# Kernel optimization log

Hardware: AMD Instinct MI355X
Metric: run time of the kernel (lower is better)

The kernel has to match this reference:

```python
import jax, jax.numpy as jnp
import numpy as np

NUM_EXPERTS = 8
HIDDEN = 2048
INTER = 5504
TOKENS = 16384  # total permuted tokens across all experts


def setup_inputs() -> dict:
    key = jax.random.key(0)
    k0, k1, k2, k3 = jax.random.split(key, 4)
    scale = 0.02  # typical init std for llama-style projections
    permuted_local_hidden_states = jax.random.normal(k0, (TOKENS, HIDDEN), jnp.float32)
    gate_w = jax.random.normal(k1, (NUM_EXPERTS, HIDDEN, INTER), jnp.float32) * scale
    up_w = jax.random.normal(k2, (NUM_EXPERTS, HIDDEN, INTER), jnp.float32) * scale
    down_w = jax.random.normal(k3, (NUM_EXPERTS, INTER, HIDDEN), jnp.float32) * scale
    tokens_per_expert = jnp.full((NUM_EXPERTS,), TOKENS // NUM_EXPERTS, jnp.int32)
    return {
        "permuted_local_hidden_states": permuted_local_hidden_states,
        "gate_w": gate_w,
        "up_w": up_w,
        "down_w": down_w,
        "tokens_per_expert": tokens_per_expert,
    }


def reference(permuted_local_hidden_states, gate_w, up_w, down_w, tokens_per_expert):
    # tokens_per_expert is uniform (TOKENS // NUM_EXPERTS each), so the
    # sequential per-expert slice loop is exactly a grouped/batched GEMM:
    # reshape tokens into [E, T_e, H] and run all experts at once.
    E = gate_w.shape[0]
    H = permuted_local_hidden_states.shape[-1]
    x = permuted_local_hidden_states.reshape(E, -1, H)  # [E, T_e, H]
    g = jnp.einsum("eth,ehi->eti", x, gate_w)           # gate proj
    u = jnp.einsum("eth,ehi->eti", x, up_w)             # up proj
    h = jax.nn.silu(g) * u                               # SwiGLU
    out = jnp.einsum("eti,eih->eth", h, down_w)         # down proj
    return out.reshape(-1, H)
```

## Files before the change

kernel.cpp:

```cpp
#include <hip/hip_runtime.h>
#include <hip/hip_bf16.h>

#define NE 8
#define HID 2048
#define INTER 5504
#define TOK 16384
#define TE 2048

typedef __bf16 bf16x8 __attribute__((ext_vector_type(8)));
typedef float f32x4 __attribute__((ext_vector_type(4)));

__device__ __forceinline__ void async_copy16(const void* g, void* l) {
    __builtin_amdgcn_global_load_lds(
        (const __attribute__((address_space(1))) void*)g,
        (__attribute__((address_space(3))) void*)l,
        16, 0, 0);
}

__device__ __forceinline__ int chunk_swz(int q) { return q ^ ((q >> 3) & 7); }

struct alignas(8) bf4 { __hip_bfloat162 a, b; };

__global__ void cast_x_kernel(const float* __restrict__ in, __hip_bfloat16* __restrict__ out) {
    size_t i = (size_t)blockIdx.x * blockDim.x + threadIdx.x;
    float4 v = reinterpret_cast<const float4*>(in)[i];
    bf4 p;
    p.a.x = __float2bfloat16(v.x);
    p.a.y = __float2bfloat16(v.y);
    p.b.x = __float2bfloat16(v.z);
    p.b.y = __float2bfloat16(v.w);
    reinterpret_cast<bf4*>(out)[i] = p;
}

__global__ void tcast_kernel(const float* __restrict__ in, __hip_bfloat16* __restrict__ out,
                             int R, int C) {
    __shared__ float tile[32][33];
    const int e = blockIdx.z;
    const int r0 = blockIdx.y * 32, c0 = blockIdx.x * 32;
    const float* src = in + (size_t)e * R * C;
    __hip_bfloat16* dst = out + (size_t)e * R * C;
    const int tx = threadIdx.x;
    const int ty = threadIdx.y;
#pragma unroll
    for (int i = 0; i < 32; i += 8)
        tile[ty + i][tx] = src[(size_t)(r0 + ty + i) * C + (c0 + tx)];
    __syncthreads();
#pragma unroll
    for (int i = 0; i < 32; i += 8)
        dst[(size_t)(c0 + ty + i) * R + (r0 + tx)] = __float2bfloat16(tile[tx][ty + i]);
}

__global__ __launch_bounds__(256, 2) void gemm1_swiglu_kernel(
    const __hip_bfloat16* __restrict__ xb,
    const __hip_bfloat16* __restrict__ gwt,
    const __hip_bfloat16* __restrict__ uwt,
    __hip_bfloat16* __restrict__ hout) {
    const int e = blockIdx.z;
    const int mt = blockIdx.x;
    const int nt = blockIdx.y;
    const int m0 = mt * 128;
    const int n0 = nt * 128;

    const __hip_bfloat16* A = xb + (size_t)(e * TE + m0) * HID;
    const __hip_bfloat16* Bg = gwt + (size_t)e * INTER * HID + (size_t)n0 * HID;
    const __hip_bfloat16* Bu = uwt + (size_t)e * INTER * HID + (size_t)n0 * HID;

    __shared__ __align__(16) __hip_bfloat16 As[128 * 32];
    __shared__ __align__(16) __hip_bfloat16 Bgs[128 * 32];
    __shared__ __align__(16) __hip_bfloat16 Bus[128 * 32];

    const int tid = threadIdx.x;
    const int wave = tid >> 6, lane = tid & 63;
    const int ch0 = wave * 128 + lane;

    const int wm = (wave >> 1) * 64;
    const int wn = (wave & 1) * 64;
    const int qd = lane >> 4;
    const int ln = lane & 15;

    f32x4 accg[4][4], accu[4][4];
    const f32x4 z4 = {0.f, 0.f, 0.f, 0.f};
#pragma unroll
    for (int mi = 0; mi < 4; ++mi)
#pragma unroll
        for (int ni = 0; ni < 4; ++ni) { accg[mi][ni] = z4; accu[mi][ni] = z4; }

    for (int kk = 0; kk < HID; kk += 32) {
#pragma unroll
        for (int i = 0; i < 2; ++i) {
            const int c = ch0 + i * 64;
            const int id = chunk_swz(c);
            const int row = id >> 2;
            const int col = (id & 3) * 8;
            async_copy16(A + (size_t)row * HID + kk + col, (void*)(As + c * 8));
            async_copy16(Bg + (size_t)row * HID + kk + col, (void*)(Bgs + c * 8));
            async_copy16(Bu + (size_t)row * HID + kk + col, (void*)(Bus + c * 8));
        }
        __syncthreads();

        bf16x8 af[4], bgf[4], buf_[4];
#pragma unroll
        for (int mi = 0; mi < 4; ++mi) {
            const int p = chunk_swz((wm + mi * 16 + ln) * 4 + qd);
            af[mi] = *reinterpret_cast<const bf16x8*>(As + p * 8);
        }
#pragma unroll
        for (int ni = 0; ni < 4; ++ni) {
            const int p = chunk_swz((wn + ni * 16 + ln) * 4 + qd);
            bgf[ni] = *reinterpret_cast<const bf16x8*>(Bgs + p * 8);
            buf_[ni] = *reinterpret_cast<const bf16x8*>(Bus + p * 8);
        }
#pragma unroll
        for (int mi = 0; mi < 4; ++mi)
#pragma unroll
            for (int ni = 0; ni < 4; ++ni) {
                accg[mi][ni] = __builtin_amdgcn_mfma_f32_16x16x32_bf16(af[mi], bgf[ni], accg[mi][ni], 0, 0, 0);
                accu[mi][ni] = __builtin_amdgcn_mfma_f32_16x16x32_bf16(af[mi], buf_[ni], accu[mi][ni], 0, 0, 0);
            }
        __syncthreads();
    }

    __hip_bfloat16* Hbase = hout + (size_t)(e * TE + m0) * INTER + n0;
#pragma unroll
    for (int mi = 0; mi < 4; ++mi)
#pragma unroll
        for (int ni = 0; ni < 4; ++ni)
#pragma unroll
            for (int r = 0; r < 4; ++r) {
                const int rr = wm + mi * 16 + qd * 4 + r;
                const int cc = wn + ni * 16 + ln;
                const float g = accg[mi][ni][r];
                const float u = accu[mi][ni][r];
                const float s = g / (1.0f + __expf(-g));
                Hbase[(size_t)rr * INTER + cc] = __float2bfloat16(s * u);
            }
}

__global__ __launch_bounds__(256, 2) void gemm2_kernel(
    const __hip_bfloat16* __restrict__ hb,
    const __hip_bfloat16* __restrict__ dwt,
    float* __restrict__ out) {
    const int e = blockIdx.z;
    const int mt = blockIdx.x;
    const int nt = blockIdx.y;
    const int m0 = mt * 128;
    const int n0 = nt * 128;

    const __hip_bfloat16* A = hb + (size_t)(e * TE + m0) * INTER;
    const __hip_bfloat16* B = dwt + (size_t)e * HID * INTER + (size_t)n0 * INTER;

    __shared__ __align__(16) __hip_bfloat16 As[128 * 32];
    __shared__ __align__(16) __hip_bfloat16 Bs[128 * 32];

    const int tid = threadIdx.x;
    const int wave = tid >> 6, lane = tid & 63;
    const int ch0 = wave * 128 + lane;

    const int wm = (wave >> 1) * 64;
    const int wn = (wave & 1) * 64;
    const int qd = lane >> 4;
    const int ln = lane & 15;

    f32x4 acc[4][4];
    const f32x4 z4 = {0.f, 0.f, 0.f, 0.f};
#pragma unroll
    for (int mi = 0; mi < 4; ++mi)
#pragma unroll
        for (int ni = 0; ni < 4; ++ni) acc[mi][ni] = z4;

    for (int kk = 0; kk < INTER; kk += 32) {
#pragma unroll
        for (int i = 0; i < 2; ++i) {
            const int c = ch0 + i * 64;
            const int id = chunk_swz(c);
            const int row = id >> 2;
            const int col = (id & 3) * 8;
            async_copy16(A + (size_t)row * INTER + kk + col, (void*)(As + c * 8));
            async_copy16(B + (size_t)row * INTER + kk + col, (void*)(Bs + c * 8));
        }
        __syncthreads();

        bf16x8 af[4], bf_[4];
#pragma unroll
        for (int mi = 0; mi < 4; ++mi) {
            const int p = chunk_swz((wm + mi * 16 + ln) * 4 + qd);
            af[mi] = *reinterpret_cast<const bf16x8*>(As + p * 8);
        }
#pragma unroll
        for (int ni = 0; ni < 4; ++ni) {
            const int p = chunk_swz((wn + ni * 16 + ln) * 4 + qd);
            bf_[ni] = *reinterpret_cast<const bf16x8*>(Bs + p * 8);
        }
#pragma unroll
        for (int mi = 0; mi < 4; ++mi)
#pragma unroll
            for (int ni = 0; ni < 4; ++ni)
                acc[mi][ni] = __builtin_amdgcn_mfma_f32_16x16x32_bf16(af[mi], bf_[ni], acc[mi][ni], 0, 0, 0);
        __syncthreads();
    }

    float* Obase = out + (size_t)(e * TE + m0) * HID + n0;
#pragma unroll
    for (int mi = 0; mi < 4; ++mi)
#pragma unroll
        for (int ni = 0; ni < 4; ++ni)
#pragma unroll
            for (int r = 0; r < 4; ++r) {
                const int rr = wm + mi * 16 + qd * 4 + r;
                const int cc = wn + ni * 16 + ln;
                Obase[(size_t)rr * HID + cc] = acc[mi][ni][r];
            }
}

extern "C" void kernel_launch(void* const* d_in, const int* in_sizes, int n_in,
                              void* d_out, int out_size, void* d_ws, size_t ws_size,
                              hipStream_t stream) {
    const float* x = (const float*)d_in[0];
    const float* gw = (const float*)d_in[1];
    const float* uw = (const float*)d_in[2];
    const float* dw = (const float*)d_in[3];
    float* out = (float*)d_out;

    const size_t XB_BYTES = (size_t)TOK * HID * 2;
    const size_t WT_BYTES = (size_t)NE * INTER * HID * 2;
    char* ws = (char*)d_ws;
    __hip_bfloat16* xb = (__hip_bfloat16*)(ws);
    __hip_bfloat16* gwt = (__hip_bfloat16*)(ws + XB_BYTES);
    __hip_bfloat16* uwt = (__hip_bfloat16*)(ws + XB_BYTES + WT_BYTES);
    __hip_bfloat16* hb = (__hip_bfloat16*)(ws + XB_BYTES + 2 * WT_BYTES);
    __hip_bfloat16* dwt = gwt;

    cast_x_kernel<<<(TOK * HID) / (256 * 4), 256, 0, stream>>>(x, xb);
    tcast_kernel<<<dim3(INTER / 32, HID / 32, NE), dim3(32, 8), 0, stream>>>(gw, gwt, HID, INTER);
    tcast_kernel<<<dim3(INTER / 32, HID / 32, NE), dim3(32, 8), 0, stream>>>(uw, uwt, HID, INTER);
    gemm1_swiglu_kernel<<<dim3(TE / 128, INTER / 128, NE), 256, 0, stream>>>(xb, gwt, uwt, hb);
    tcast_kernel<<<dim3(HID / 32, INTER / 32, NE), dim3(32, 8), 0, stream>>>(dw, dwt, INTER, HID);
    gemm2_kernel<<<dim3(TE / 128, HID / 128, NE), 256, 0, stream>>>(hb, dwt, out);
}
```

Baseline: 2.435 ms.

## Rewrite GEMMs with 256x256 tiles, 4-stage LDS pipeline, tile swizzle, wider transpose-cast

Both GEMM kernels move to 512-thread blocks with larger 256-row tiles and a four-buffer async global-to-LDS pipeline that prefetches two K-steps ahead. Loads are split across two half-steps, with raw s_barrier plus waitcnt replacing __syncthreads, and setprio raised around the MFMA bursts. Block indices are remapped so consecutive workgroups cover the same expert and weight tile, aiming at better L2 reuse. The transpose-cast kernel now packs pairs of bf16 values and writes 16-byte vectors, cutting the cost of the weight conversion passes. Risks are higher register pressure from the larger accumulator sets and the correctness of the hand-tuned waitcnt and barrier placement.

```diff
diff --git a/kernel.cpp b/kernel.cpp
--- a/kernel.cpp
+++ b/kernel.cpp
@@ -18,6 +18,12 @@
 }
 
 __device__ __forceinline__ int chunk_swz(int q) { return q ^ ((q >> 3) & 7); }
+
+__device__ __forceinline__ void block_barrier() {
+    asm volatile("" ::: "memory");
+    __builtin_amdgcn_s_barrier();
+    asm volatile("" ::: "memory");
+}
 
 struct alignas(8) bf4 { __hip_bfloat162 a, b; };
 
@@ -32,183 +38,290 @@
     reinterpret_cast<bf4*>(out)[i] = p;
 }
 
-__global__ void tcast_kernel(const float* __restrict__ in, __hip_bfloat16* __restrict__ out,
-                             int R, int C) {
-    __shared__ float tile[32][33];
+__global__ __launch_bounds__(256) void tcast2_kernel(const float* __restrict__ in,
+                                                     __hip_bfloat16* __restrict__ out,
+                                                     int R, int C) {
+    __shared__ unsigned int D[32][129];
     const int e = blockIdx.z;
-    const int r0 = blockIdx.y * 32, c0 = blockIdx.x * 32;
+    const int r0 = blockIdx.y * 64, c0 = blockIdx.x * 128;
     const float* src = in + (size_t)e * R * C;
     __hip_bfloat16* dst = out + (size_t)e * R * C;
-    const int tx = threadIdx.x;
-    const int ty = threadIdx.y;
-#pragma unroll
-    for (int i = 0; i < 32; i += 8)
-        tile[ty + i][tx] = src[(size_t)(r0 + ty + i) * C + (c0 + tx)];
+    const int tid = threadIdx.x;
+
+#pragma unroll
+    for (int it = 0; it < 16; ++it) {
+        const int idx = tid + it * 256;
+        const int rp = idx >> 7, c = idx & 127;
+        const float lo = src[(size_t)(r0 + 2 * rp) * C + (c0 + c)];
+        const float hi = src[(size_t)(r0 + 2 * rp + 1) * C + (c0 + c)];
+        const unsigned short a = __builtin_bit_cast(unsigned short, __float2bfloat16(lo));
+        const unsigned short b = __builtin_bit_cast(unsigned short, __float2bfloat16(hi));
+        D[rp][c] = (unsigned)a | ((unsigned)b << 16);
+    }
     __syncthreads();
 #pragma unroll
-    for (int i = 0; i < 32; i += 8)
-        dst[(size_t)(c0 + ty + i) * R + (r0 + tx)] = __float2bfloat16(tile[tx][ty + i]);
-}
-
-__global__ __launch_bounds__(256, 2) void gemm1_swiglu_kernel(
+    for (int it = 0; it < 4; ++it) {
+        const int idx = tid + it * 256;
+        const int c = idx >> 3, q = idx & 7;
+        uint4 w;
+        w.x = D[4 * q + 0][c];
+        w.y = D[4 * q + 1][c];
+        w.z = D[4 * q + 2][c];
+        w.w = D[4 * q + 3][c];
+        *reinterpret_cast<uint4*>(dst + (size_t)(c0 + c) * R + r0 + q * 8) = w;
+    }
+}
+
+__global__ __launch_bounds__(512, 2) void gemm1_swiglu_kernel(
     const __hip_bfloat16* __restrict__ xb,
     const __hip_bfloat16* __restrict__ gwt,
     const __hip_bfloat16* __restrict__ uwt,
     __hip_bfloat16* __restrict__ hout) {
-    const int e = blockIdx.z;
-    const int mt = blockIdx.x;
-    const int nt = blockIdx.y;
-    const int m0 = mt * 128;
-    const int n0 = nt * 128;
+    const int lin = blockIdx.x + ((blockIdx.y + blockIdx.z * 43) << 3);
+    const int swz = (lin & 7) * 344 + (lin >> 3);
+    const int e = swz / 344;
+    const int rem = swz - e * 344;
+    const int nt = rem >> 3, mt = rem & 7;
+    const int m0 = mt * 256, n0 = nt * 128;
 
     const __hip_bfloat16* A = xb + (size_t)(e * TE + m0) * HID;
     const __hip_bfloat16* Bg = gwt + (size_t)e * INTER * HID + (size_t)n0 * HID;
     const __hip_bfloat16* Bu = uwt + (size_t)e * INTER * HID + (size_t)n0 * HID;
 
-    __shared__ __align__(16) __hip_bfloat16 As[128 * 32];
-    __shared__ __align__(16) __hip_bfloat16 Bgs[128 * 32];
-    __shared__ __align__(16) __hip_bfloat16 Bus[128 * 32];
+    __shared__ __align__(16) __hip_bfloat16 S[4 * 2048 * 8];
 
     const int tid = threadIdx.x;
     const int wave = tid >> 6, lane = tid & 63;
-    const int ch0 = wave * 128 + lane;
-
-    const int wm = (wave >> 1) * 64;
-    const int wn = (wave & 1) * 64;
-    const int qd = lane >> 4;
-    const int ln = lane & 15;
-
-    f32x4 accg[4][4], accu[4][4];
+    const int wmh = (wave >> 2) * 128;
+    const int wnq = (wave & 3) * 32;
+    const int qd = lane >> 4, ln = lane & 15;
+
+    const __hip_bfloat16* aSrc[2];
+    const __hip_bfloat16* bSrc[2];
+#pragma unroll
+    for (int p = 0; p < 2; ++p) {
+        const int c = p * 512 + tid;
+        const int id = chunk_swz(c);
+        const int row = id >> 2, col = (id & 3) * 8;
+        aSrc[p] = A + (size_t)row * HID + col;
+        bSrc[p] = (row < 128 ? Bg + (size_t)row * HID
+                             : Bu + (size_t)(row - 128) * HID) + col;
+    }
+
+    int pA[8], pG[2], pU[2];
+#pragma unroll
+    for (int mi = 0; mi < 8; ++mi) pA[mi] = chunk_swz((wmh + mi * 16 + ln) * 4 + qd);
+#pragma unroll
+    for (int ni = 0; ni < 2; ++ni) {
+        pG[ni] = 1024 + chunk_swz((wnq + ni * 16 + ln) * 4 + qd);
+        pU[ni] = 1024 + chunk_swz((128 + wnq + ni * 16 + ln) * 4 + qd);
+    }
+
+    f32x4 accg[8][2], accu[8][2];
     const f32x4 z4 = {0.f, 0.f, 0.f, 0.f};
 #pragma unroll
-    for (int mi = 0; mi < 4; ++mi)
-#pragma unroll
-        for (int ni = 0; ni < 4; ++ni) { accg[mi][ni] = z4; accu[mi][ni] = z4; }
-
-    for (int kk = 0; kk < HID; kk += 32) {
-#pragma unroll
-        for (int i = 0; i < 2; ++i) {
-            const int c = ch0 + i * 64;
-            const int id = chunk_swz(c);
-            const int row = id >> 2;
-            const int col = (id & 3) * 8;
-            async_copy16(A + (size_t)row * HID + kk + col, (void*)(As + c * 8));
-            async_copy16(Bg + (size_t)row * HID + kk + col, (void*)(Bgs + c * 8));
-            async_copy16(Bu + (size_t)row * HID + kk + col, (void*)(Bus + c * 8));
-        }
-        __syncthreads();
-
-        bf16x8 af[4], bgf[4], buf_[4];
-#pragma unroll
-        for (int mi = 0; mi < 4; ++mi) {
-            const int p = chunk_swz((wm + mi * 16 + ln) * 4 + qd);
-            af[mi] = *reinterpret_cast<const bf16x8*>(As + p * 8);
-        }
-#pragma unroll
-        for (int ni = 0; ni < 4; ++ni) {
-            const int p = chunk_swz((wn + ni * 16 + ln) * 4 + qd);
-            bgf[ni] = *reinterpret_cast<const bf16x8*>(Bgs + p * 8);
-            buf_[ni] = *reinterpret_cast<const bf16x8*>(Bus + p * 8);
-        }
-#pragma unroll
-        for (int mi = 0; mi < 4; ++mi)
-#pragma unroll
-            for (int ni = 0; ni < 4; ++ni) {
-                accg[mi][ni] = __builtin_amdgcn_mfma_f32_16x16x32_bf16(af[mi], bgf[ni], accg[mi][ni], 0, 0, 0);
-                accu[mi][ni] = __builtin_amdgcn_mfma_f32_16x16x32_bf16(af[mi], buf_[ni], accu[mi][ni], 0, 0, 0);
+    for (int mi = 0; mi < 8; ++mi)
+#pragma unroll
+        for (int ni = 0; ni < 2; ++ni) { accg[mi][ni] = z4; accu[mi][ni] = z4; }
+
+    const int NT = HID / 32;
+#pragma unroll
+    for (int t = 0; t < 2; ++t)
+#pragma unroll
+        for (int p = 0; p < 2; ++p) {
+            const int c = p * 512 + tid;
+            async_copy16(aSrc[p] + t * 32, (void*)(S + (size_t)(t * 2048 + c) * 8));
+            async_copy16(bSrc[p] + t * 32, (void*)(S + (size_t)(t * 2048 + 1024 + c) * 8));
+        }
+
+    for (int t = 0; t < NT; ++t) {
+        const __hip_bfloat16* Sb = S + (size_t)((t & 3) * 2048) * 8;
+        const int buf2 = ((t + 2) & 3) * 2048;
+        const int k2 = (t + 2 < NT ? t + 2 : t + 2 - NT) * 32;
+
+        {
+            const int c = tid;
+            async_copy16(aSrc[0] + k2, (void*)(S + (size_t)(buf2 + c) * 8));
+            async_copy16(bSrc[0] + k2, (void*)(S + (size_t)(buf2 + 1024 + c) * 8));
+        }
+        asm volatile("s_waitcnt vmcnt(6)" ::: "memory");
+        block_barrier();
+
+        bf16x8 bg[2], bu[2], af[4];
+#pragma unroll
+        for (int ni = 0; ni < 2; ++ni) {
+            bg[ni] = *reinterpret_cast<const bf16x8*>(Sb + (size_t)pG[ni] * 8);
+            bu[ni] = *reinterpret_cast<const bf16x8*>(Sb + (size_t)pU[ni] * 8);
+        }
+#pragma unroll
+        for (int mi = 0; mi < 4; ++mi)
+            af[mi] = *reinterpret_cast<const bf16x8*>(Sb + (size_t)pA[mi] * 8);
+
+        __builtin_amdgcn_s_setprio(1);
+#pragma unroll
+        for (int mi = 0; mi < 4; ++mi)
+#pragma unroll
+            for (int ni = 0; ni < 2; ++ni) {
+                accg[mi][ni] = __builtin_amdgcn_mfma_f32_16x16x32_bf16(af[mi], bg[ni], accg[mi][ni], 0, 0, 0);
+                accu[mi][ni] = __builtin_amdgcn_mfma_f32_16x16x32_bf16(af[mi], bu[ni], accu[mi][ni], 0, 0, 0);
             }
-        __syncthreads();
-    }
-
-    __hip_bfloat16* Hbase = hout + (size_t)(e * TE + m0) * INTER + n0;
-#pragma unroll
-    for (int mi = 0; mi < 4; ++mi)
-#pragma unroll
-        for (int ni = 0; ni < 4; ++ni)
+        __builtin_amdgcn_s_setprio(0);
+        block_barrier();
+
+        {
+            const int c = 512 + tid;
+            async_copy16(aSrc[1] + k2, (void*)(S + (size_t)(buf2 + c) * 8));
+            async_copy16(bSrc[1] + k2, (void*)(S + (size_t)(buf2 + 1024 + c) * 8));
+        }
+        bf16x8 af2[4];
+#pragma unroll
+        for (int mi = 0; mi < 4; ++mi)
+            af2[mi] = *reinterpret_cast<const bf16x8*>(Sb + (size_t)pA[mi + 4] * 8);
+
+        __builtin_amdgcn_s_setprio(1);
+#pragma unroll
+        for (int mi = 0; mi < 4; ++mi)
+#pragma unroll
+            for (int ni = 0; ni < 2; ++ni) {
+                accg[mi + 4][ni] = __builtin_amdgcn_mfma_f32_16x16x32_bf16(af2[mi], bg[ni], accg[mi + 4][ni], 0, 0, 0);
+                accu[mi + 4][ni] = __builtin_amdgcn_mfma_f32_16x16x32_bf16(af2[mi], bu[ni], accu[mi + 4][ni], 0, 0, 0);
+            }
+        __builtin_amdgcn_s_setprio(0);
+        block_barrier();
+    }
+
+    __hip_bfloat16* H = hout + (size_t)(e * TE + m0 + wmh) * INTER + n0 + wnq;
+#pragma unroll
+    for (int mi = 0; mi < 8; ++mi)
+#pragma unroll
+        for (int ni = 0; ni < 2; ++ni)
 #pragma unroll
             for (int r = 0; r < 4; ++r) {
-                const int rr = wm + mi * 16 + qd * 4 + r;
-                const int cc = wn + ni * 16 + ln;
+                const int rr = mi * 16 + qd * 4 + r;
+                const int cc = ni * 16 + ln;
                 const float g = accg[mi][ni][r];
                 const float u = accu[mi][ni][r];
                 const float s = g / (1.0f + __expf(-g));
-                Hbase[(size_t)rr * INTER + cc] = __float2bfloat16(s * u);
+                H[(size_t)rr * INTER + cc] = __float2bfloat16(s * u);
             }
 }
 
-__global__ __launch_bounds__(256, 2) void gemm2_kernel(
+__global__ __launch_bounds__(512, 2) void gemm2_kernel(
     const __hip_bfloat16* __restrict__ hb,
     const __hip_bfloat16* __restrict__ dwt,
     float* __restrict__ out) {
-    const int e = blockIdx.z;
-    const int mt = blockIdx.x;
-    const int nt = blockIdx.y;
-    const int m0 = mt * 128;
-    const int n0 = nt * 128;
+    const int lin = blockIdx.x + ((blockIdx.y + (blockIdx.z << 3)) << 3);
+    const int swz = (lin & 7) * 64 + (lin >> 3);
+    const int e = swz >> 6;
+    const int rem = swz & 63;
+    const int nt = rem >> 3, mt = rem & 7;
+    const int m0 = mt * 256, n0 = nt * 256;
 
     const __hip_bfloat16* A = hb + (size_t)(e * TE + m0) * INTER;
     const __hip_bfloat16* B = dwt + (size_t)e * HID * INTER + (size_t)n0 * INTER;
 
-    __shared__ __align__(16) __hip_bfloat16 As[128 * 32];
-    __shared__ __align__(16) __hip_bfloat16 Bs[128 * 32];
+    __shared__ __align__(16) __hip_bfloat16 S[4 * 2048 * 8];
 
     const int tid = threadIdx.x;
     const int wave = tid >> 6, lane = tid & 63;
-    const int ch0 = wave * 128 + lane;
-
-    const int wm = (wave >> 1) * 64;
-    const int wn = (wave & 1) * 64;
-    const int qd = lane >> 4;
-    const int ln = lane & 15;
-
-    f32x4 acc[4][4];
+    const int wmh = (wave >> 2) * 128;
+    const int wnq = (wave & 3) * 64;
+    const int qd = lane >> 4, ln = lane & 15;
+
+    const __hip_bfloat16* aSrc[2];
+    const __hip_bfloat16* bSrc[2];
+#pragma unroll
+    for (int p = 0; p < 2; ++p) {
+        const int c = p * 512 + tid;
+        const int id = chunk_swz(c);
+        const int row = id >> 2, col = (id & 3) * 8;
+        aSrc[p] = A + (size_t)row * INTER + col;
+        bSrc[p] = B + (size_t)row * INTER + col;
+    }
+
+    int pA[8], pB[4];
+#pragma unroll
+    for (int mi = 0; mi < 8; ++mi) pA[mi] = chunk_swz((wmh + mi * 16 + ln) * 4 + qd);
+#pragma unroll
+    for (int ni = 0; ni < 4; ++ni) pB[ni] = 1024 + chunk_swz((wnq + ni * 16 + ln) * 4 + qd);
+
+    f32x4 acc[8][4];
     const f32x4 z4 = {0.f, 0.f, 0.f, 0.f};
 #pragma unroll
-    for (int mi = 0; mi < 4; ++mi)
+    for (int mi = 0; mi < 8; ++mi)
 #pragma unroll
         for (int ni = 0; ni < 4; ++ni) acc[mi][ni] = z4;
 
-    for (int kk = 0; kk < INTER; kk += 32) {
-#pragma unroll
-        for (int i = 0; i < 2; ++i) {
-            const int c = ch0 + i * 64;
-            const int id = chunk_swz(c);
-            const int row = id >> 2;
-            const int col = (id & 3) * 8;
-            async_copy16(A + (size_t)row * INTER + kk + col, (void*)(As + c * 8));
-            async_copy16(B + (size_t)row * INTER + kk + col, (void*)(Bs + c * 8));
-        }
-        __syncthreads();
-
-        bf16x8 af[4], bf_[4];
-#pragma unroll
-        for (int mi = 0; mi < 4; ++mi) {
-            const int p = chunk_swz((wm + mi * 16 + ln) * 4 + qd);
-            af[mi] = *reinterpret_cast<const bf16x8*>(As + p * 8);
-        }
-#pragma unroll
-        for (int ni = 0; ni < 4; ++ni) {
-            const int p = chunk_swz((wn + ni * 16 + ln) * 4 + qd);
-            bf_[ni] = *reinterpret_cast<const bf16x8*>(Bs + p * 8);
-        }
+    const int NT = INTER / 32;
+#pragma unroll
+    for (int t = 0; t < 2; ++t)
+#pragma unroll
+        for (int p = 0; p < 2; ++p) {
+            const int c = p * 512 + tid;
+            async_copy16(aSrc[p] + t * 32, (void*)(S + (size_t)(t * 2048 + c) * 8));
+            async_copy16(bSrc[p] + t * 32, (void*)(S + (size_t)(t * 2048 + 1024 + c) * 8));
+        }
+
+    for (int t = 0; t < NT; ++t) {
+        const __hip_bfloat16* Sb = S + (size_t)((t & 3) * 2048) * 8;
+        const int buf2 = ((t + 2) & 3) * 2048;
+        const int k2 = (t + 2 < NT ? t + 2 : t + 2 - NT) * 32;
+
+        {
+            const int c = tid;
+            async_copy16(aSrc[0] + k2, (void*)(S + (size_t)(buf2 + c) * 8));
+            async_copy16(bSrc[0] + k2, (void*)(S + (size_t)(buf2 + 1024 + c) * 8));
+        }
+        asm volatile("s_waitcnt vmcnt(6)" ::: "memory");
+        block_barrier();
+
+        bf16x8 bf_[4], af[4];
+#pragma unroll
+        for (int ni = 0; ni < 4; ++ni)
+            bf_[ni] = *reinterpret_cast<const bf16x8*>(Sb + (size_t)pB[ni] * 8);
+#pragma unroll
+        for (int mi = 0; mi < 4; ++mi)
+            af[mi] = *reinterpret_cast<const bf16x8*>(Sb + (size_t)pA[mi] * 8);
+
+        __builtin_amdgcn_s_setprio(1);
 #pragma unroll
         for (int mi = 0; mi < 4; ++mi)
 #pragma unroll
             for (int ni = 0; ni < 4; ++ni)
                 acc[mi][ni] = __builtin_amdgcn_mfma_f32_16x16x32_bf16(af[mi], bf_[ni], acc[mi][ni], 0, 0, 0);
-        __syncthreads();
-    }
-
-    float* Obase = out + (size_t)(e * TE + m0) * HID + n0;
-#pragma unroll
-    for (int mi = 0; mi < 4; ++mi)
+        __builtin_amdgcn_s_setprio(0);
+        block_barrier();
+
+        {
+            const int c = 512 + tid;
+            async_copy16(aSrc[1] + k2, (void*)(S + (size_t)(buf2 + c) * 8));
+            async_copy16(bSrc[1] + k2, (void*)(S + (size_t)(buf2 + 1024 + c) * 8));
+        }
+        bf16x8 af2[4];
+#pragma unroll
+        for (int mi = 0; mi < 4; ++mi)
+            af2[mi] = *reinterpret_cast<const bf16x8*>(Sb + (size_t)pA[mi + 4] * 8);
+
+        __builtin_amdgcn_s_setprio(1);
+#pragma unroll
+        for (int mi = 0; mi < 4; ++mi)
+#pragma unroll
+            for (int ni = 0; ni < 4; ++ni)
+                acc[mi + 4][ni] = __builtin_amdgcn_mfma_f32_16x16x32_bf16(af2[mi], bf_[ni], acc[mi + 4][ni], 0, 0, 0);
+        __builtin_amdgcn_s_setprio(0);
+        block_barrier();
+    }
+
+    float* O = out + (size_t)(e * TE + m0 + wmh) * HID + n0 + wnq;
+#pragma unroll
+    for (int mi = 0; mi < 8; ++mi)
 #pragma unroll
         for (int ni = 0; ni < 4; ++ni)
 #pragma unroll
             for (int r = 0; r < 4; ++r) {
-                const int rr = wm + mi * 16 + qd * 4 + r;
-                const int cc = wn + ni * 16 + ln;
-                Obase[(size_t)rr * HID + cc] = acc[mi][ni][r];
+                const int rr = mi * 16 + qd * 4 + r;
+                const int cc = ni * 16 + ln;
+                O[(size_t)rr * HID + cc] = acc[mi][ni][r];
             }
 }
 
@@ -231,9 +344,9 @@
     __hip_bfloat16* dwt = gwt;
 
     cast_x_kernel<<<(TOK * HID) / (256 * 4), 256, 0, stream>>>(x, xb);
-    tcast_kernel<<<dim3(INTER / 32, HID / 32, NE), dim3(32, 8), 0, stream>>>(gw, gwt, HID, INTER);
-    tcast_kernel<<<dim3(INTER / 32, HID / 32, NE), dim3(32, 8), 0, stream>>>(uw, uwt, HID, INTER);
-    gemm1_swiglu_kernel<<<dim3(TE / 128, INTER / 128, NE), 256, 0, stream>>>(xb, gwt, uwt, hb);
-    tcast_kernel<<<dim3(HID / 32, INTER / 32, NE), dim3(32, 8), 0, stream>>>(dw, dwt, INTER, HID);
-    gemm2_kernel<<<dim3(TE / 128, HID / 128, NE), 256, 0, stream>>>(hb, dwt, out);
-}
+    tcast2_kernel<<<dim3(INTER / 128, HID / 64, NE), 256, 0, stream>>>(gw, gwt, HID, INTER);
+    tcast2_kernel<<<dim3(INTER / 128, HID / 64, NE), 256, 0, stream>>>(uw, uwt, HID, INTER);
+    gemm1_swiglu_kernel<<<dim3(TE / 256, INTER / 128, NE), 512, 0, stream>>>(xb, gwt, uwt, hb);
+    tcast2_kernel<<<dim3(HID / 128, INTER / 64, NE), 256, 0, stream>>>(dw, dwt, INTER, HID);
+    gemm2_kernel<<<dim3(TE / 256, HID / 256, NE), 512, 0, stream>>>(hb, dwt, out);
+}
```

Measured after the change: 2.085 ms. 1.17x faster.
